# Optimization experiments

Measured on AMD Instinct MI355X. Metric: run time of the kernel, lower is better.

## Reference

```python
import jax, jax.numpy as jnp
import numpy as np

B, T, D, H = 2, 2048, 2048, 32
HD = D // H
# quantization scales (constructor-time attributes in the original repo)
A_PROJ = 3e-4   # q/k/v proj alpha (W8A8B8O8Linear)
A_QK = 2e-5     # qk_bmm alpha (BMM_S8T_S8N_F32T)
A_PV = 1e-2     # pv_bmm alpha (BMM_S8T_S8N_S8T)
A_OUT = 1e-4    # out_proj alpha (W8A8BFP32OFP32Linear)


def _i8(key, shape):
    return jax.random.randint(key, shape, -128, 128, dtype=jnp.int32).astype(jnp.int8)


def setup_inputs() -> dict:
    key = jax.random.key(0)
    ks = jax.random.split(key, 10)
    hidden_states = _i8(ks[0], (B, T, D))
    # causal mask, 0 on/below diagonal, large negative above
    causal = jnp.triu(jnp.full((T, T), -1e9, dtype=jnp.float32), k=1)
    attention_mask = jnp.broadcast_to(causal, (B, 1, T, T))
    return {
        "hidden_states": hidden_states,
        "attention_mask": attention_mask,
        "Wq": _i8(ks[1], (D, D)), "bq": _i8(ks[2], (D,)),
        "Wk": _i8(ks[3], (D, D)), "bk": _i8(ks[4], (D,)),
        "Wv": _i8(ks[5], (D, D)), "bv": _i8(ks[6], (D,)),
        "Wo": _i8(ks[7], (D, D)),
        "bo": jax.random.normal(ks[8], (D,), dtype=jnp.float32),
    }


def _w8a8b8o8(x_i8, W_i8, b_i8, alpha):
    # int8 GEMM -> int32 accum; epilogue: alpha*acc + bias, saturate to int8
    acc = jnp.einsum('btk,nk->btn', x_i8.astype(jnp.int32), W_i8.astype(jnp.int32))
    y = alpha * acc.astype(jnp.float32) + b_i8.astype(jnp.float32)
    return jnp.clip(jnp.round(y), -128, 127).astype(jnp.int8)


def reference(hidden_states, attention_mask, Wq, bq, Wk, bk, Wv, bv, Wo, bo):
    # q/k/v projections: int8 in, int8 out
    q = _w8a8b8o8(hidden_states, Wq, bq, A_PROJ)
    k = _w8a8b8o8(hidden_states, Wk, bk, A_PROJ)
    v = _w8a8b8o8(hidden_states, Wv, bv, A_PROJ)

    def shape(x):  # [B,T,D] -> [B,H,T,HD]
        return x.reshape(B, T, H, HD).transpose(0, 2, 1, 3)

    qh, kh, vh = shape(q), shape(k), shape(v)

    # qk_bmm (BMM_S8T_S8N_F32T): fp32 = alpha * int8 q @ k^T
    attn = A_QK * jnp.einsum('bhtd,bhsd->bhts',
                             qh.astype(jnp.int32), kh.astype(jnp.int32)).astype(jnp.float32)
    attn = attn + attention_mask  # [B,1,T,T] broadcasts over heads
    attn = jnp.maximum(attn, jnp.finfo(jnp.float32).min)
    probs = jax.nn.softmax(attn, axis=-1)

    # quantize probs: p.mul_(127).round_() -> int8
    p_i8 = jnp.clip(jnp.round(probs * 127.0), -128, 127).astype(jnp.int8)

    # pv_bmm (BMM_S8T_S8N_S8T): int8 out = sat(round(alpha * p @ v))
    pv = jnp.einsum('bhts,bhsd->bhtd', p_i8.astype(jnp.int32), vh.astype(jnp.int32))
    attn_out_i8 = jnp.clip(jnp.round(A_PV * pv.astype(jnp.float32)), -128, 127).astype(jnp.int8)

    # [B,H,T,HD] -> [B,T,D]
    attn_out = attn_out_i8.transpose(0, 2, 1, 3).reshape(B, T, D)

    # out_proj (W8A8BFP32OFP32Linear): fp32 = alpha*(x@W^T) + fp32 bias
    acc = jnp.einsum('btk,nk->btn', attn_out.astype(jnp.int32), Wo.astype(jnp.int32))
    out = A_OUT * acc.astype(jnp.float32) + bo
    return out
```

## Files before the change

kernel.cpp:

```cpp
#include <hip/hip_runtime.h>
#include <cstdint>

#define A_PROJ 3e-4f
#define A_QK   2e-5f
#define A_PV   1e-2f
#define A_OUT  1e-4f

#define NB 2
#define NT 2048
#define ND 2048
#define NH 32
#define NHD 64
#define NM (NB*NT)

typedef int v4i __attribute__((ext_vector_type(4)));

__device__ __forceinline__ int8_t sat8(float y) {
  float r = rintf(y);
  r = fminf(fmaxf(r, -128.f), 127.f);
  return (int8_t)(int)r;
}

__device__ __forceinline__ float exp2_fast(float x) {
  return __builtin_amdgcn_exp2f(x);
}

__device__ __forceinline__ void gl2lds16(const int8_t* g, int8_t* l) {
  __builtin_amdgcn_global_load_lds(
      (const __attribute__((address_space(1))) void*)g,
      (__attribute__((address_space(3))) void*)l, 16, 0, 0);
}

__device__ __forceinline__ uint32_t pack_lo4(float f0, float f1, float f2, float f3) {
  uint32_t u0 = __float_as_uint(f0), u1 = __float_as_uint(f1);
  uint32_t u2 = __float_as_uint(f2), u3 = __float_as_uint(f3);
  uint32_t lo = __builtin_amdgcn_perm(u1, u0, 0x04000400u);
  uint32_t hi = __builtin_amdgcn_perm(u3, u2, 0x04000400u);
  return __builtin_amdgcn_perm(hi, lo, 0x05040100u);
}

#define NWW (ND*ND/4)
__global__ void pack_all(const int* __restrict__ X,
                         const int* __restrict__ W0, const int* __restrict__ W1,
                         const int* __restrict__ W2, const int* __restrict__ W3,
                         int8_t* __restrict__ dX, int8_t* __restrict__ dW0,
                         int8_t* __restrict__ dW1, int8_t* __restrict__ dW2,
                         int8_t* __restrict__ dW3) {
  int i = blockIdx.x * blockDim.x + threadIdx.x;
  const int nx = NM*ND/4;
  const int* src; int8_t* dst; int off;
  if (i < nx) { src = X; dst = dX; off = i; }
  else {
    int j = i - nx;
    int r = j >> 20;
    off = j & (NWW - 1);
    src = (r == 0) ? W0 : (r == 1) ? W1 : (r == 2) ? W2 : W3;
    dst = (r == 0) ? dW0 : (r == 1) ? dW1 : (r == 2) ? dW2 : dW3;
  }
  int4 v = ((const int4*)src)[off];
  uint32_t p = (uint32_t)(v.x & 255) | ((uint32_t)(v.y & 255) << 8) |
               ((uint32_t)(v.z & 255) << 16) | ((uint32_t)(v.w & 255) << 24);
  ((uint32_t*)dst)[off] = p;
}

__global__ __launch_bounds__(256) void gemm_qkv(
    const int8_t* __restrict__ X,
    const int8_t* __restrict__ Wq, const int8_t* __restrict__ Wk, const int8_t* __restrict__ Wv,
    const int* __restrict__ bq, const int* __restrict__ bk, const int* __restrict__ bv,
    int8_t* __restrict__ Qh, int8_t* __restrict__ Kh, int8_t* __restrict__ Vt)
{
  __shared__ __align__(16) int8_t As[2][128][64];
  __shared__ __align__(16) int8_t Bs[2][128][64];
  const int z = blockIdx.z;
  const int8_t* W  = (z == 0) ? Wq : ((z == 1) ? Wk : Wv);
  const int* bias  = (z == 0) ? bq : ((z == 1) ? bk : bv);
  const int m0 = blockIdx.x * 128, n0 = blockIdx.y * 128;
  const int tid = threadIdx.x, lane = tid & 63, wave = tid >> 6;
  const int wm = wave >> 1, wn = wave & 1;
  const int l15 = lane & 15, quad = lane >> 4;

  const int srow = lane >> 2;
  const int scol = (((lane & 3) ^ ((lane >> 3) & 3)) * 16);
  const int rqcol = (quad ^ ((l15 >> 1) & 3)) * 16;

  const int8_t* srcp[4];
  int8_t* dstp[4];
  #pragma unroll
  for (int j = 0; j < 4; ++j) {
    int slot = j * 4 + wave;
    int rblk = slot & 7;
    int row = rblk * 16 + srow;
    if (slot < 8) { srcp[j] = &X[(size_t)(m0 + row) * ND + scol]; dstp[j] = &As[0][rblk*16][0]; }
    else          { srcp[j] = &W[(size_t)(n0 + row) * ND + scol]; dstp[j] = &Bs[0][rblk*16][0]; }
  }

  v4i acc[4][4];
  const v4i vzero = {0, 0, 0, 0};
  #pragma unroll
  for (int i = 0; i < 4; ++i)
    #pragma unroll
    for (int j = 0; j < 4; ++j) acc[i][j] = vzero;

  #pragma unroll
  for (int j = 0; j < 4; ++j) gl2lds16(srcp[j], dstp[j]);
  __syncthreads();

  int cur = 0;
  for (int k0 = 64; k0 <= ND; k0 += 64) {
    if (k0 < ND) {
      const int boff = (cur ^ 1) * 128 * 64;
      #pragma unroll
      for (int j = 0; j < 4; ++j) gl2lds16(srcp[j] + k0, dstp[j] + boff);
    }
    v4i a[4], b[4];
    #pragma unroll
    for (int mt = 0; mt < 4; ++mt) a[mt] = *(const v4i*)&As[cur][wm*64 + mt*16 + l15][rqcol];
    #pragma unroll
    for (int nt = 0; nt < 4; ++nt) b[nt] = *(const v4i*)&Bs[cur][wn*64 + nt*16 + l15][rqcol];
    #pragma unroll
    for (int mt = 0; mt < 4; ++mt)
      #pragma unroll
      for (int nt = 0; nt < 4; ++nt)
        acc[mt][nt] = __builtin_amdgcn_mfma_i32_16x16x64_i8(a[mt], b[nt], acc[mt][nt], 0, 0, 0);
    __syncthreads();
    cur ^= 1;
  }

  float bf[4];
  #pragma unroll
  for (int nt = 0; nt < 4; ++nt) bf[nt] = (float)bias[n0 + wn*64 + nt*16 + l15];

  if (z == 2) {
    #pragma unroll
    for (int mt = 0; mt < 4; ++mt)
      #pragma unroll
      for (int nt = 0; nt < 4; ++nt) {
        int tbase = (m0 + wm*64 + mt*16 + quad*4) & (NT - 1);
        int bb = (m0 + wm*64) >> 11;
        int n = n0 + wn*64 + nt*16 + l15;
        int hh = n >> 6, hd = n & (NHD - 1);
        uint32_t pk = 0;
        #pragma unroll
        for (int r = 0; r < 4; ++r) {
          uint32_t q = (uint32_t)(uint8_t)sat8(A_PROJ * (float)acc[mt][nt][r] + bf[nt]);
          pk |= q << (8 * r);
        }
        size_t bh = (size_t)bb * NH + hh;
        *(uint32_t*)&Vt[(bh * NHD + hd) * NT + tbase] = pk;
      }
  } else {
    int8_t* O = (z == 0) ? Qh : Kh;
    #pragma unroll
    for (int mt = 0; mt < 4; ++mt)
      #pragma unroll
      for (int nt = 0; nt < 4; ++nt)
        #pragma unroll
        for (int r = 0; r < 4; ++r) {
          int m = m0 + wm*64 + mt*16 + quad*4 + r;
          int n = n0 + wn*64 + nt*16 + l15;
          int8_t q = sat8(A_PROJ * (float)acc[mt][nt][r] + bf[nt]);
          int bb = m >> 11, t = m & (NT - 1);
          int hh = n >> 6, hd = n & (NHD - 1);
          size_t bh = (size_t)bb * NH + hh;
          O[(bh * NT + t) * NHD + hd] = q;
        }
  }
}

__global__ __launch_bounds__(512, 8) void attn_fused(
    const int8_t* __restrict__ Qh, const int8_t* __restrict__ Kh, const int8_t* __restrict__ Vt,
    int8_t* __restrict__ AO)
{
  __shared__ __align__(16) int8_t Ksd[2][64][64];
  __shared__ __align__(16) int8_t Vsd[2][64][64];
  __shared__ __align__(16) uint32_t Ps32[8][16][20];

  const int bx = blockIdx.x;
  const int bh = blockIdx.y;
  const int tid = threadIdx.x, lane = tid & 63, wave = tid >> 6;
  const int l15 = lane & 15, quad = lane >> 4;
  const v4i vzero = {0, 0, 0, 0};
  const float MAGIC = 12582912.0f;
  const float C2 = 2.8853900817779268e-05f;

  const int jg = bh >> 4;
  const int x = (jg == 0) ? bx : (jg == 1) ? (15 - bx)
              : (jg == 2) ? ((bx + 8) & 15) : ((7 - bx) & 15);

  const int8_t* Qp = Qh + (size_t)bh * NT * NHD;
  const int8_t* Kp = Kh + (size_t)bh * NT * NHD;
  const int8_t* Vp = Vt + (size_t)bh * NHD * NT;
  const int bb = bh >> 5, hhead = bh & (NH - 1);

  const int t0 = x * 128;
  const int nsteps = 2 * x + 2;
  const int tw = t0 + wave * 16;
  const int tme = tw + l15;

  const int strow = lane >> 2;
  const int stcol = (((lane & 3) ^ ((lane >> 3) & 3)) * 16);
  const int fcol  = (quad ^ ((l15 >> 1) & 3)) * 16;

  v4i qf = *(const v4i*)&Qp[(size_t)(tw + l15) * NHD + quad * 16];

  float ls0 = 0.f, ls1 = 0.f, ls2 = 0.f, ls3 = 0.f;
  if (wave < 4)
    gl2lds16(&Kp[(size_t)(0 + wave*16 + strow) * NHD + stcol], &Ksd[0][wave*16][0]);
  __syncthreads();
  int cur = 0;
  for (int st = 0; st < nsteps; ++st) {
    if (st + 1 < nsteps && wave < 4)
      gl2lds16(&Kp[(size_t)((st+1)*64 + wave*16 + strow) * NHD + stcol],
               &Ksd[cur ^ 1][wave*16][0]);
    const int s0 = st * 64;
    if (s0 <= tw + 15) {
      v4i kf[4];
      #pragma unroll
      for (int mt = 0; mt < 4; ++mt) kf[mt] = *(const v4i*)&Ksd[cur][mt*16 + l15][fcol];
      if (s0 + 63 <= tw) {
        #pragma unroll
        for (int mt = 0; mt < 4; ++mt) {
          v4i sa = __builtin_amdgcn_mfma_i32_16x16x64_i8(kf[mt], qf, vzero, 0, 0, 0);
          ls0 += exp2_fast(C2 * (float)sa[0]);
          ls1 += exp2_fast(C2 * (float)sa[1]);
          ls2 += exp2_fast(C2 * (float)sa[2]);
          ls3 += exp2_fast(C2 * (float)sa[3]);
        }
      } else {
        #pragma unroll
        for (int mt = 0; mt < 4; ++mt) {
          v4i sa = __builtin_amdgcn_mfma_i32_16x16x64_i8(kf[mt], qf, vzero, 0, 0, 0);
          const int sb = s0 + mt*16 + quad*4;
          ls0 += (sb + 0 <= tme) ? exp2_fast(C2 * (float)sa[0]) : 0.f;
          ls1 += (sb + 1 <= tme) ? exp2_fast(C2 * (float)sa[1]) : 0.f;
          ls2 += (sb + 2 <= tme) ? exp2_fast(C2 * (float)sa[2]) : 0.f;
          ls3 += (sb + 3 <= tme) ? exp2_fast(C2 * (float)sa[3]) : 0.f;
        }
      }
    }
    __syncthreads();
    cur ^= 1;
  }
  float lsum = (ls0 + ls1) + (ls2 + ls3);
  lsum += __shfl_xor(lsum, 16, 64);
  lsum += __shfl_xor(lsum, 32, 64);
  const float linv = 127.0f / lsum;

  v4i accv[4];
  #pragma unroll
  for (int jj = 0; jj < 4; ++jj) accv[jj] = vzero;

  if (wave < 4)
    gl2lds16(&Kp[(size_t)(0 + wave*16 + strow) * NHD + stcol], &Ksd[0][wave*16][0]);
  else
    gl2lds16(&Vp[(size_t)((wave-4)*16 + strow) * NT + 0 + stcol], &Vsd[0][(wave-4)*16][0]);
  __syncthreads();
  cur = 0;
  for (int st = 0; st < nsteps; ++st) {
    if (st + 1 < nsteps) {
      if (wave < 4)
        gl2lds16(&Kp[(size_t)((st+1)*64 + wave*16 + strow) * NHD + stcol],
                 &Ksd[cur ^ 1][wave*16][0]);
      else
        gl2lds16(&Vp[(size_t)((wave-4)*16 + strow) * NT + (st+1)*64 + stcol],
                 &Vsd[cur ^ 1][(wave-4)*16][0]);
    }
    const int s0 = st * 64;
    if (s0 <= tw + 15) {
      v4i kf[4];
      #pragma unroll
      for (int mt = 0; mt < 4; ++mt) kf[mt] = *(const v4i*)&Ksd[cur][mt*16 + l15][fcol];
      if (s0 + 63 <= tw) {
        #pragma unroll
        for (int mt = 0; mt < 4; ++mt) {
          v4i sa = __builtin_amdgcn_mfma_i32_16x16x64_i8(kf[mt], qf, vzero, 0, 0, 0);
          float f0 = fmaf(exp2_fast(C2 * (float)sa[0]), linv, MAGIC);
          float f1 = fmaf(exp2_fast(C2 * (float)sa[1]), linv, MAGIC);
          float f2 = fmaf(exp2_fast(C2 * (float)sa[2]), linv, MAGIC);
          float f3 = fmaf(exp2_fast(C2 * (float)sa[3]), linv, MAGIC);
          Ps32[wave][l15][mt*4 + quad] = pack_lo4(f0, f1, f2, f3);
        }
      } else {
        #pragma unroll
        for (int mt = 0; mt < 4; ++mt) {
          v4i sa = __builtin_amdgcn_mfma_i32_16x16x64_i8(kf[mt], qf, vzero, 0, 0, 0);
          const int sb = s0 + mt*16 + quad*4;
          float e0 = (sb + 0 <= tme) ? exp2_fast(C2 * (float)sa[0]) : 0.f;
          float e1 = (sb + 1 <= tme) ? exp2_fast(C2 * (float)sa[1]) : 0.f;
          float e2 = (sb + 2 <= tme) ? exp2_fast(C2 * (float)sa[2]) : 0.f;
          float e3 = (sb + 3 <= tme) ? exp2_fast(C2 * (float)sa[3]) : 0.f;
          Ps32[wave][l15][mt*4 + quad] =
              pack_lo4(fmaf(e0, linv, MAGIC), fmaf(e1, linv, MAGIC),
                       fmaf(e2, linv, MAGIC), fmaf(e3, linv, MAGIC));
        }
      }
      v4i ap = *(const v4i*)&Ps32[wave][l15][quad*4];
      #pragma unroll
      for (int nt2 = 0; nt2 < 4; ++nt2) {
        v4i bvv = *(const v4i*)&Vsd[cur][nt2*16 + l15][fcol];
        accv[nt2] = __builtin_amdgcn_mfma_i32_16x16x64_i8(ap, bvv, accv[nt2], 0, 0, 0);
      }
    }
    __syncthreads();
    cur ^= 1;
  }

  #pragma unroll
  for (int nt2 = 0; nt2 < 4; ++nt2)
    #pragma unroll
    for (int r = 0; r < 4; ++r) {
      int t = tw + quad*4 + r;
      int d = nt2*16 + l15;
      AO[((size_t)bb * NT + t) * ND + hhead * NHD + d] = sat8(A_PV * (float)accv[nt2][r]);
    }
}

__global__ __launch_bounds__(256) void gemm_out(
    const int8_t* __restrict__ X, const int8_t* __restrict__ W,
    const float* __restrict__ bo, float* __restrict__ out)
{
  __shared__ __align__(16) int8_t As[2][128][64];
  __shared__ __align__(16) int8_t Bs[2][128][64];
  const int m0 = blockIdx.x * 128, n0 = blockIdx.y * 128;
  const int tid = threadIdx.x, lane = tid & 63, wave = tid >> 6;
  const int wm = wave >> 1, wn = wave & 1;
  const int l15 = lane & 15, quad = lane >> 4;
  const int srow = lane >> 2;
  const int scol = (((lane & 3) ^ ((lane >> 3) & 3)) * 16);
  const int rqcol = (quad ^ ((l15 >> 1) & 3)) * 16;

  const int8_t* srcp[4];
  int8_t* dstp[4];
  #pragma unroll
  for (int j = 0; j < 4; ++j) {
    int slot = j * 4 + wave;
    int rblk = slot & 7;
    int row = rblk * 16 + srow;
    if (slot < 8) { srcp[j] = &X[(size_t)(m0 + row) * ND + scol]; dstp[j] = &As[0][rblk*16][0]; }
    else          { srcp[j] = &W[(size_t)(n0 + row) * ND + scol]; dstp[j] = &Bs[0][rblk*16][0]; }
  }

  v4i acc[4][4];
  const v4i vzero = {0, 0, 0, 0};
  #pragma unroll
  for (int i = 0; i < 4; ++i)
    #pragma unroll
    for (int j = 0; j < 4; ++j) acc[i][j] = vzero;

  #pragma unroll
  for (int j = 0; j < 4; ++j) gl2lds16(srcp[j], dstp[j]);
  __syncthreads();

  int cur = 0;
  for (int k0 = 64; k0 <= ND; k0 += 64) {
    if (k0 < ND) {
      const int boff = (cur ^ 1) * 128 * 64;
      #pragma unroll
      for (int j = 0; j < 4; ++j) gl2lds16(srcp[j] + k0, dstp[j] + boff);
    }
    v4i a[4], b[4];
    #pragma unroll
    for (int mt = 0; mt < 4; ++mt) a[mt] = *(const v4i*)&As[cur][wm*64 + mt*16 + l15][rqcol];
    #pragma unroll
    for (int nt = 0; nt < 4; ++nt) b[nt] = *(const v4i*)&Bs[cur][wn*64 + nt*16 + l15][rqcol];
    #pragma unroll
    for (int mt = 0; mt < 4; ++mt)
      #pragma unroll
      for (int nt = 0; nt < 4; ++nt)
        acc[mt][nt] = __builtin_amdgcn_mfma_i32_16x16x64_i8(a[mt], b[nt], acc[mt][nt], 0, 0, 0);
    __syncthreads();
    cur ^= 1;
  }

  float bf[4];
  #pragma unroll
  for (int nt = 0; nt < 4; ++nt) bf[nt] = bo[n0 + wn*64 + nt*16 + l15];

  #pragma unroll
  for (int mt = 0; mt < 4; ++mt)
    #pragma unroll
    for (int nt = 0; nt < 4; ++nt)
      #pragma unroll
      for (int r = 0; r < 4; ++r) {
        int m = m0 + wm*64 + mt*16 + quad*4 + r;
        int n = n0 + wn*64 + nt*16 + l15;
        out[(size_t)m * ND + n] = A_OUT * (float)acc[mt][nt][r] + bf[nt];
      }
}

extern "C" void kernel_launch(void* const* d_in, const int* in_sizes, int n_in,
                              void* d_out, int out_size, void* d_ws, size_t ws_size,
                              hipStream_t stream)
{
  const int*   hs  = (const int*)d_in[0];
  const int*   Wq  = (const int*)d_in[2];
  const int*   bq  = (const int*)d_in[3];
  const int*   Wk  = (const int*)d_in[4];
  const int*   bkb = (const int*)d_in[5];
  const int*   Wv  = (const int*)d_in[6];
  const int*   bvb = (const int*)d_in[7];
  const int*   Wo  = (const int*)d_in[8];
  const float* bo  = (const float*)d_in[9];
  float* out = (float*)d_out;

  char* ws = (char*)d_ws;
  const size_t SZ_X = (size_t)NM * ND;
  const size_t SZ_W = (size_t)ND * ND;
  const size_t SZ_H = (size_t)NB * NH * NT * NHD;
  int8_t* Xp  = (int8_t*)ws;
  int8_t* Wqp = (int8_t*)(ws + SZ_X);
  int8_t* Wkp = Wqp + SZ_W;
  int8_t* Wvp = Wkp + SZ_W;
  int8_t* Wop = Wvp + SZ_W;
  int8_t* Qh  = Wop + SZ_W;
  int8_t* Kh  = Qh + SZ_H;
  int8_t* Vt  = Kh + SZ_H;
  int8_t* AO  = Xp;

  const int ntot = (int)(SZ_X/4 + 4 * (SZ_W/4));
  pack_all<<<(ntot + 255) / 256, 256, 0, stream>>>(hs, Wq, Wk, Wv, Wo,
                                                   Xp, Wqp, Wkp, Wvp, Wop);

  gemm_qkv<<<dim3(NM/128, ND/128, 3), 256, 0, stream>>>(Xp, Wqp, Wkp, Wvp, bq, bkb, bvb, Qh, Kh, Vt);
  attn_fused<<<dim3(16, NB*NH), 512, 0, stream>>>(Qh, Kh, Vt, AO);
  gemm_out<<<dim3(NM/128, ND/128), 256, 0, stream>>>(AO, Wop, bo, out);
}
```

Measured before the change: 312.2 us.

## Triple-buffer LDS in QKV and output GEMMs with vmcnt-based waits

Both int8 GEMM kernels go from double-buffered to triple-buffered shared-memory tiles and prefetch two K-steps ahead. The full __syncthreads after each step is replaced by a partial s_waitcnt vmcnt(4) plus a single s_barrier at the top of the loop. The goal is to keep more global-to-LDS loads in flight so memory latency overlaps the MFMA work, with one barrier per iteration instead of two. In exchange, LDS per block grows from 32KB to 48KB, which may lower occupancy. Correctness now depends on the vmcnt count matching the four async loads issued per stage.

Result: slower. 331.7 us (+6.3%).

```diff
diff --git a/kernel.cpp b/kernel.cpp
--- a/kernel.cpp
+++ b/kernel.cpp
@@ -69,8 +69,8 @@
     const int* __restrict__ bq, const int* __restrict__ bk, const int* __restrict__ bv,
     int8_t* __restrict__ Qh, int8_t* __restrict__ Kh, int8_t* __restrict__ Vt)
 {
-  __shared__ __align__(16) int8_t As[2][128][64];
-  __shared__ __align__(16) int8_t Bs[2][128][64];
+  __shared__ __align__(16) int8_t As[3][128][64];
+  __shared__ __align__(16) int8_t Bs[3][128][64];
   const int z = blockIdx.z;
   const int8_t* W  = (z == 0) ? Wq : ((z == 1) ? Wk : Wv);
   const int* bias  = (z == 0) ? bq : ((z == 1) ? bk : bv);
@@ -103,27 +103,38 @@
 
   #pragma unroll
   for (int j = 0; j < 4; ++j) gl2lds16(srcp[j], dstp[j]);
-  __syncthreads();
-
-  int cur = 0;
-  for (int k0 = 64; k0 <= ND; k0 += 64) {
-    if (k0 < ND) {
-      const int boff = (cur ^ 1) * 128 * 64;
-      #pragma unroll
-      for (int j = 0; j < 4; ++j) gl2lds16(srcp[j] + k0, dstp[j] + boff);
-    }
+  #pragma unroll
+  for (int j = 0; j < 4; ++j) gl2lds16(srcp[j] + 64, dstp[j] + 8192);
+
+  const int NK = ND / 64;
+  int cb = 0, sb = 2;
+  for (int t = 0; t < NK; ++t) {
+    if (t < NK - 1) {
+      asm volatile("s_waitcnt vmcnt(4)" ::: "memory");
+    } else {
+      asm volatile("s_waitcnt vmcnt(0)" ::: "memory");
+    }
+    __builtin_amdgcn_s_barrier();
+    if (t + 2 < NK) {
+      const int boff = sb * 8192;
+      const int goff = (t + 2) * 64;
+      #pragma unroll
+      for (int j = 0; j < 4; ++j) gl2lds16(srcp[j] + goff, dstp[j] + boff);
+    }
+    const int8_t* Ab = &As[0][0][0] + cb * 8192;
+    const int8_t* Bb = &Bs[0][0][0] + cb * 8192;
     v4i a[4], b[4];
     #pragma unroll
-    for (int mt = 0; mt < 4; ++mt) a[mt] = *(const v4i*)&As[cur][wm*64 + mt*16 + l15][rqcol];
-    #pragma unroll
-    for (int nt = 0; nt < 4; ++nt) b[nt] = *(const v4i*)&Bs[cur][wn*64 + nt*16 + l15][rqcol];
+    for (int mt = 0; mt < 4; ++mt) a[mt] = *(const v4i*)(Ab + (wm*64 + mt*16 + l15)*64 + rqcol);
+    #pragma unroll
+    for (int nt = 0; nt < 4; ++nt) b[nt] = *(const v4i*)(Bb + (wn*64 + nt*16 + l15)*64 + rqcol);
     #pragma unroll
     for (int mt = 0; mt < 4; ++mt)
       #pragma unroll
       for (int nt = 0; nt < 4; ++nt)
         acc[mt][nt] = __builtin_amdgcn_mfma_i32_16x16x64_i8(a[mt], b[nt], acc[mt][nt], 0, 0, 0);
-    __syncthreads();
-    cur ^= 1;
+    cb = (cb == 2) ? 0 : cb + 1;
+    sb = (sb == 2) ? 0 : sb + 1;
   }
 
   float bf[4];
@@ -319,8 +330,8 @@
     const int8_t* __restrict__ X, const int8_t* __restrict__ W,
     const float* __restrict__ bo, float* __restrict__ out)
 {
-  __shared__ __align__(16) int8_t As[2][128][64];
-  __shared__ __align__(16) int8_t Bs[2][128][64];
+  __shared__ __align__(16) int8_t As[3][128][64];
+  __shared__ __align__(16) int8_t Bs[3][128][64];
   const int m0 = blockIdx.x * 128, n0 = blockIdx.y * 128;
   const int tid = threadIdx.x, lane = tid & 63, wave = tid >> 6;
   const int wm = wave >> 1, wn = wave & 1;
@@ -349,27 +360,38 @@
 
   #pragma unroll
   for (int j = 0; j < 4; ++j) gl2lds16(srcp[j], dstp[j]);
-  __syncthreads();
-
-  int cur = 0;
-  for (int k0 = 64; k0 <= ND; k0 += 64) {
-    if (k0 < ND) {
-      const int boff = (cur ^ 1) * 128 * 64;
-      #pragma unroll
-      for (int j = 0; j < 4; ++j) gl2lds16(srcp[j] + k0, dstp[j] + boff);
-    }
+  #pragma unroll
+  for (int j = 0; j < 4; ++j) gl2lds16(srcp[j] + 64, dstp[j] + 8192);
+
+  const int NK = ND / 64;
+  int cb = 0, sb = 2;
+  for (int t = 0; t < NK; ++t) {
+    if (t < NK - 1) {
+      asm volatile("s_waitcnt vmcnt(4)" ::: "memory");
+    } else {
+      asm volatile("s_waitcnt vmcnt(0)" ::: "memory");
+    }
+    __builtin_amdgcn_s_barrier();
+    if (t + 2 < NK) {
+      const int boff = sb * 8192;
+      const int goff = (t + 2) * 64;
+      #pragma unroll
+      for (int j = 0; j < 4; ++j) gl2lds16(srcp[j] + goff, dstp[j] + boff);
+    }
+    const int8_t* Ab = &As[0][0][0] + cb * 8192;
+    const int8_t* Bb = &Bs[0][0][0] + cb * 8192;
     v4i a[4], b[4];
     #pragma unroll
-    for (int mt = 0; mt < 4; ++mt) a[mt] = *(const v4i*)&As[cur][wm*64 + mt*16 + l15][rqcol];
-    #pragma unroll
-    for (int nt = 0; nt < 4; ++nt) b[nt] = *(const v4i*)&Bs[cur][wn*64 + nt*16 + l15][rqcol];
+    for (int mt = 0; mt < 4; ++mt) a[mt] = *(const v4i*)(Ab + (wm*64 + mt*16 + l15)*64 + rqcol);
+    #pragma unroll
+    for (int nt = 0; nt < 4; ++nt) b[nt] = *(const v4i*)(Bb + (wn*64 + nt*16 + l15)*64 + rqcol);
     #pragma unroll
     for (int mt = 0; mt < 4; ++mt)
       #pragma unroll
       for (int nt = 0; nt < 4; ++nt)
         acc[mt][nt] = __builtin_amdgcn_mfma_i32_16x16x64_i8(a[mt], b[nt], acc[mt][nt], 0, 0, 0);
-    __syncthreads();
-    cur ^= 1;
+    cb = (cb == 2) ? 0 : cb + 1;
+    sb = (sb == 2) ? 0 : sb + 1;
   }
 
   float bf[4];
```

## Enlarge QKV GEMM tile to 256x256 with 8 waves per block

Applied to the files above, without the earlier changes.

The fused QKV projection GEMM now uses 256x256 output tiles computed by 512 threads (2x4 waves), each wave owning a 128x64 sub-tile. The aim is more data reuse per byte loaded into shared memory and fewer redundant global loads of X and the weights. The cost is a grid of 16x8x3 = 384 blocks, which may underfill the GPU's compute units or leave a partial wave. Each thread also holds twice as many accumulators, and shared memory per block doubles, both of which reduce occupancy.

Result: slower. 338.1 us (+8.3%).

```diff
diff --git a/kernel.cpp b/kernel.cpp
--- a/kernel.cpp
+++ b/kernel.cpp
@@ -63,20 +63,20 @@
   ((uint32_t*)dst)[off] = p;
 }
 
-__global__ __launch_bounds__(256) void gemm_qkv(
+__global__ __launch_bounds__(512, 1) void gemm_qkv(
     const int8_t* __restrict__ X,
     const int8_t* __restrict__ Wq, const int8_t* __restrict__ Wk, const int8_t* __restrict__ Wv,
     const int* __restrict__ bq, const int* __restrict__ bk, const int* __restrict__ bv,
     int8_t* __restrict__ Qh, int8_t* __restrict__ Kh, int8_t* __restrict__ Vt)
 {
-  __shared__ __align__(16) int8_t As[2][128][64];
-  __shared__ __align__(16) int8_t Bs[2][128][64];
+  __shared__ __align__(16) int8_t As[2][256][64];
+  __shared__ __align__(16) int8_t Bs[2][256][64];
   const int z = blockIdx.z;
   const int8_t* W  = (z == 0) ? Wq : ((z == 1) ? Wk : Wv);
   const int* bias  = (z == 0) ? bq : ((z == 1) ? bk : bv);
-  const int m0 = blockIdx.x * 128, n0 = blockIdx.y * 128;
+  const int m0 = blockIdx.x * 256, n0 = blockIdx.y * 256;
   const int tid = threadIdx.x, lane = tid & 63, wave = tid >> 6;
-  const int wm = wave >> 1, wn = wave & 1;
+  const int wm = wave >> 2, wn = wave & 3;
   const int l15 = lane & 15, quad = lane >> 4;
 
   const int srow = lane >> 2;
@@ -85,19 +85,15 @@
 
   const int8_t* srcp[4];
   int8_t* dstp[4];
-  #pragma unroll
-  for (int j = 0; j < 4; ++j) {
-    int slot = j * 4 + wave;
-    int rblk = slot & 7;
-    int row = rblk * 16 + srow;
-    if (slot < 8) { srcp[j] = &X[(size_t)(m0 + row) * ND + scol]; dstp[j] = &As[0][rblk*16][0]; }
-    else          { srcp[j] = &W[(size_t)(n0 + row) * ND + scol]; dstp[j] = &Bs[0][rblk*16][0]; }
-  }
-
-  v4i acc[4][4];
+  srcp[0] = &X[(size_t)(m0 +       wave*16 + srow) * ND + scol]; dstp[0] = &As[0][      wave*16][0];
+  srcp[1] = &X[(size_t)(m0 + 128 + wave*16 + srow) * ND + scol]; dstp[1] = &As[0][128 + wave*16][0];
+  srcp[2] = &W[(size_t)(n0 +       wave*16 + srow) * ND + scol]; dstp[2] = &Bs[0][      wave*16][0];
+  srcp[3] = &W[(size_t)(n0 + 128 + wave*16 + srow) * ND + scol]; dstp[3] = &Bs[0][128 + wave*16][0];
+
+  v4i acc[8][4];
   const v4i vzero = {0, 0, 0, 0};
   #pragma unroll
-  for (int i = 0; i < 4; ++i)
+  for (int i = 0; i < 8; ++i)
     #pragma unroll
     for (int j = 0; j < 4; ++j) acc[i][j] = vzero;
 
@@ -106,22 +102,27 @@
   __syncthreads();
 
   int cur = 0;
-  for (int k0 = 64; k0 <= ND; k0 += 64) {
-    if (k0 < ND) {
-      const int boff = (cur ^ 1) * 128 * 64;
-      #pragma unroll
-      for (int j = 0; j < 4; ++j) gl2lds16(srcp[j] + k0, dstp[j] + boff);
-    }
-    v4i a[4], b[4];
-    #pragma unroll
-    for (int mt = 0; mt < 4; ++mt) a[mt] = *(const v4i*)&As[cur][wm*64 + mt*16 + l15][rqcol];
-    #pragma unroll
-    for (int nt = 0; nt < 4; ++nt) b[nt] = *(const v4i*)&Bs[cur][wn*64 + nt*16 + l15][rqcol];
-    #pragma unroll
-    for (int mt = 0; mt < 4; ++mt)
+  const int NK = ND / 64;
+  for (int t = 0; t < NK; ++t) {
+    if (t + 1 < NK) {
+      const int boff = (cur ^ 1) * 16384;
+      const int goff = (t + 1) * 64;
+      #pragma unroll
+      for (int j = 0; j < 4; ++j) gl2lds16(srcp[j] + goff, dstp[j] + boff);
+    }
+    const int8_t* Ab = &As[cur][0][0];
+    const int8_t* Bb = &Bs[cur][0][0];
+    v4i b[4];
+    #pragma unroll
+    for (int nt = 0; nt < 4; ++nt)
+      b[nt] = *(const v4i*)(Bb + (wn*64 + nt*16 + l15) * 64 + rqcol);
+    #pragma unroll
+    for (int mt = 0; mt < 8; ++mt) {
+      v4i a = *(const v4i*)(Ab + (wm*128 + mt*16 + l15) * 64 + rqcol);
       #pragma unroll
       for (int nt = 0; nt < 4; ++nt)
-        acc[mt][nt] = __builtin_amdgcn_mfma_i32_16x16x64_i8(a[mt], b[nt], acc[mt][nt], 0, 0, 0);
+        acc[mt][nt] = __builtin_amdgcn_mfma_i32_16x16x64_i8(a, b[nt], acc[mt][nt], 0, 0, 0);
+    }
     __syncthreads();
     cur ^= 1;
   }
@@ -132,11 +133,11 @@
 
   if (z == 2) {
     #pragma unroll
-    for (int mt = 0; mt < 4; ++mt)
+    for (int mt = 0; mt < 8; ++mt)
       #pragma unroll
       for (int nt = 0; nt < 4; ++nt) {
-        int tbase = (m0 + wm*64 + mt*16 + quad*4) & (NT - 1);
-        int bb = (m0 + wm*64) >> 11;
+        int tbase = (m0 + wm*128 + mt*16 + quad*4) & (NT - 1);
+        int bb = (m0 + wm*128) >> 11;
         int n = n0 + wn*64 + nt*16 + l15;
         int hh = n >> 6, hd = n & (NHD - 1);
         uint32_t pk = 0;
@@ -151,12 +152,12 @@
   } else {
     int8_t* O = (z == 0) ? Qh : Kh;
     #pragma unroll
-    for (int mt = 0; mt < 4; ++mt)
+    for (int mt = 0; mt < 8; ++mt)
       #pragma unroll
       for (int nt = 0; nt < 4; ++nt)
         #pragma unroll
         for (int r = 0; r < 4; ++r) {
-          int m = m0 + wm*64 + mt*16 + quad*4 + r;
+          int m = m0 + wm*128 + mt*16 + quad*4 + r;
           int n = n0 + wn*64 + nt*16 + l15;
           int8_t q = sat8(A_PROJ * (float)acc[mt][nt][r] + bf[nt]);
           int bb = m >> 11, t = m & (NT - 1);
@@ -354,7 +355,7 @@
   int cur = 0;
   for (int k0 = 64; k0 <= ND; k0 += 64) {
     if (k0 < ND) {
-      const int boff = (cur ^ 1) * 128 * 64;
+      const int boff = (cur ^ 1) * 8192;
       #pragma unroll
       for (int j = 0; j < 4; ++j) gl2lds16(srcp[j] + k0, dstp[j] + boff);
     }
@@ -421,7 +422,7 @@
   pack_all<<<(ntot + 255) / 256, 256, 0, stream>>>(hs, Wq, Wk, Wv, Wo,
                                                    Xp, Wqp, Wkp, Wvp, Wop);
 
-  gemm_qkv<<<dim3(NM/128, ND/128, 3), 256, 0, stream>>>(Xp, Wqp, Wkp, Wvp, bq, bkb, bvb, Qh, Kh, Vt);
+  gemm_qkv<<<dim3(NM/256, ND/256, 3), 512, 0, stream>>>(Xp, Wqp, Wkp, Wvp, bq, bkb, bvb, Qh, Kh, Vt);
   attn_fused<<<dim3(16, NB*NH), 512, 0, stream>>>(Qh, Kh, Vt, AO);
   gemm_out<<<dim3(NM/128, ND/128), 256, 0, stream>>>(AO, Wop, bo, out);
 }
```
